# Kernel optimization log

Hardware: AMD Instinct MI355X
Metric: run time of the kernel (lower is better)

## Reference

```python
import jax, jax.numpy as jnp
import numpy as np

D = 64
H = 2          # n_heads
HD = D // H    # head_dim = 32
EPS = 1e-5


def _layer_norm(x, gamma, beta):
    mu = jnp.mean(x, axis=-1, keepdims=True)
    var = jnp.var(x, axis=-1, keepdims=True)
    return (x - mu) * jax.lax.rsqrt(var + EPS) * gamma + beta


def setup_inputs() -> dict:
    key = jax.random.key(0)
    ks = jax.random.split(key, 12)
    s = 0.05
    n_stocks, tau = 512, 512
    return {
        "x":     jax.random.normal(ks[0], (n_stocks, tau, D), dtype=jnp.float32),
        "Wqkv":  jax.random.normal(ks[1], (3 * D, D), dtype=jnp.float32) * s,
        "bqkv":  jax.random.normal(ks[2], (3 * D,), dtype=jnp.float32) * s,
        "Wo":    jax.random.normal(ks[3], (D, D), dtype=jnp.float32) * s,
        "bo":    jax.random.normal(ks[4], (D,), dtype=jnp.float32) * s,
        "g1":    jnp.ones((D,), dtype=jnp.float32),
        "beta1": jnp.zeros((D,), dtype=jnp.float32),
        "W1":    jax.random.normal(ks[5], (4 * D, D), dtype=jnp.float32) * s,
        "bf1":   jax.random.normal(ks[6], (4 * D,), dtype=jnp.float32) * s,
        "W2":    jax.random.normal(ks[7], (D, 4 * D), dtype=jnp.float32) * s,
        "bf2":   jax.random.normal(ks[8], (D,), dtype=jnp.float32) * s,
        "g2":    jnp.ones((D,), dtype=jnp.float32),
        "beta2": jnp.zeros((D,), dtype=jnp.float32),
    }


def reference(x, Wqkv, bqkv, Wo, bo, g1, beta1, W1, bf1, W2, bf2, g2, beta2):
    # x: (n_stocks, tau, D). The torch loop over tau == batched attention with
    # batch = tau, seq = n_stocks. Dropout is identity (eval mode).
    n_stocks, tau, d = x.shape
    Ht = jnp.transpose(x, (1, 0, 2))                    # (tau, S, D)

    qkv = Ht @ Wqkv.T + bqkv                            # (tau, S, 3D)
    q, k, v = jnp.split(qkv, 3, axis=-1)
    q = q.reshape(tau, n_stocks, H, HD)
    k = k.reshape(tau, n_stocks, H, HD)
    v = v.reshape(tau, n_stocks, H, HD)

    scores = jnp.einsum("bqhd,bkhd->bhqk", q, k) / jnp.sqrt(jnp.float32(HD))
    attn = jax.nn.softmax(scores, axis=-1)              # (tau, H, S, S)
    ctx = jnp.einsum("bhqk,bkhd->bqhd", attn, v).reshape(tau, n_stocks, D)
    attn_out = ctx @ Wo.T + bo                          # (tau, S, D)

    y = _layer_norm(attn_out + Ht, g1, beta1)           # residual + LN1
    ffn = jax.nn.relu(y @ W1.T + bf1) @ W2.T + bf2      # (tau, S, D)
    z = _layer_norm(ffn + y, g2, beta2)                 # residual + LN2

    return jnp.transpose(z, (1, 0, 2))                  # (n_stocks, tau, D)
```

## Files before the change

### kernel.cpp

```cpp
#include <hip/hip_runtime.h>
#include <hip/hip_bf16.h>
#include <cmath>

#define NS 512
#define NT 512
#define DIM 64
#define HD 32

typedef __attribute__((ext_vector_type(8))) short short8;
typedef __attribute__((ext_vector_type(16))) float f32x16;

union FragU { unsigned w[4]; short8 f; };

__device__ __forceinline__ float fexp2(float x) {
  float r; asm("v_exp_f32 %0, %1" : "=v"(r) : "v"(x)); return r;
}

__device__ __forceinline__ unsigned short bfbits(float x) {
  __hip_bfloat16 h = __float2bfloat16(x);
  return __builtin_bit_cast(unsigned short, h);
}
__device__ __forceinline__ unsigned pk2(float lo, float hi) {
  return (unsigned)bfbits(lo) | ((unsigned)bfbits(hi) << 16);
}
__device__ __forceinline__ float lo_f(unsigned w) { return __uint_as_float(w << 16); }
__device__ __forceinline__ float hi_f(unsigned w) { return __uint_as_float(w & 0xffff0000u); }
__device__ __forceinline__ short8 ldg8(const __hip_bfloat16* p) {
  return *reinterpret_cast<const short8*>(p);
}

__device__ __forceinline__ void pl32swap(unsigned& a, unsigned& b) {
  asm volatile("v_permlane32_swap_b32 %0, %1" : "+v"(a), "+v"(b));
}

__device__ __forceinline__ void repack(const float* p, short8& o1, short8& o2) {
  unsigned pk[8];
  #pragma unroll
  for (int j = 0; j < 8; ++j) pk[j] = pk2(p[2 * j], p[2 * j + 1]);
  pl32swap(pk[0], pk[2]);
  pl32swap(pk[1], pk[3]);
  pl32swap(pk[4], pk[6]);
  pl32swap(pk[5], pk[7]);
  FragU a1, a2;
  a1.w[0] = pk[0]; a1.w[1] = pk[1]; a1.w[2] = pk[2]; a1.w[3] = pk[3];
  a2.w[0] = pk[4]; a2.w[1] = pk[5]; a2.w[2] = pk[6]; a2.w[3] = pk[7];
  o1 = a1.f; o2 = a2.f;
}

__global__ void k_cvt(const float* __restrict__ Wqkv, const float* __restrict__ Wo,
                      const float* __restrict__ W1, const float* __restrict__ W2,
                      __hip_bfloat16* __restrict__ dst) {
  int i = blockIdx.x * 256 + threadIdx.x;
  float v;
  if (i < 12288) v = Wqkv[i];
  else if (i < 16384) v = Wo[i - 12288];
  else if (i < 32768) v = W1[i - 16384];
  else v = W2[i - 32768];
  dst[i] = __float2bfloat16(v);
}

__global__ __launch_bounds__(512, 4) void k_attn(
    const float* __restrict__ x, const __hip_bfloat16* __restrict__ Wb,
    const float* __restrict__ bqkv, __hip_bfloat16* __restrict__ ctx) {
  __shared__ char smem[65536];
  const int t = blockIdx.x, h = blockIdx.y;
  const int tid = threadIdx.x;
  const int l = tid & 63, wv = tid >> 6, hi = l >> 5, l31 = l & 31;

  short8 xf[2][4];
  #pragma unroll
  for (int rt = 0; rt < 2; ++rt) {
    int row = wv * 64 + rt * 32 + l31;
    const float* xr = x + ((size_t)row * NT + t) * DIM + hi * 8;
    #pragma unroll
    for (int st = 0; st < 4; ++st) {
      float4 f0 = *reinterpret_cast<const float4*>(xr + st * 16);
      float4 f1 = *reinterpret_cast<const float4*>(xr + st * 16 + 4);
      FragU fu;
      fu.w[0] = pk2(f0.x, f0.y); fu.w[1] = pk2(f0.z, f0.w);
      fu.w[2] = pk2(f1.x, f1.y); fu.w[3] = pk2(f1.z, f1.w);
      xf[rt][st] = fu.f;
    }
  }

  {
    short8 wkb[4];
    #pragma unroll
    for (int st = 0; st < 4; ++st)
      wkb[st] = ldg8(Wb + (size_t)(64 + h * 32 + l31) * 64 + st * 16 + hi * 8);
    #pragma unroll
    for (int rt = 0; rt < 2; ++rt) {
      f32x16 ka = {};
      #pragma unroll
      for (int st = 0; st < 4; ++st)
        ka = __builtin_amdgcn_mfma_f32_32x32x16_bf16(wkb[st], xf[rt][st], ka, 0, 0, 0);
      int stock = wv * 64 + rt * 32 + l31;
      char* kb = smem + stock * 64 + (hi << 3);
      #pragma unroll
      for (int rq = 0; rq < 4; ++rq) {
        uint2 d2 = make_uint2(pk2(ka[4 * rq + 0], ka[4 * rq + 1]),
                              pk2(ka[4 * rq + 2], ka[4 * rq + 3]));
        *reinterpret_cast<uint2*>(kb + ((rq ^ ((stock >> 1) & 3)) << 4)) = d2;
      }
    }
  }

  {
    short8 wvb[4];
    #pragma unroll
    for (int st = 0; st < 4; ++st)
      wvb[st] = ldg8(Wb + (size_t)(128 + h * 32 + l31) * 64 + st * 16 + hi * 8);
    #pragma unroll
    for (int rt = 0; rt < 2; ++rt) {
      f32x16 va = {};
      #pragma unroll
      for (int st = 0; st < 4; ++st)
        va = __builtin_amdgcn_mfma_f32_32x32x16_bf16(xf[rt][st], wvb[st], va, 0, 0, 0);
      #pragma unroll
      for (int g = 0; g < 4; ++g) {
        int kb = wv * 64 + rt * 32 + g * 8 + hi * 4;
        uint2 d2 = make_uint2(pk2(va[4 * g + 0], va[4 * g + 1]),
                              pk2(va[4 * g + 2], va[4 * g + 3]));
        *reinterpret_cast<uint2*>(
            smem + 32768 + l31 * 1024 + (((kb >> 3) ^ (l31 & 7)) << 4) + ((kb & 7) << 1)) = d2;
      }
    }
  }

  short8 qfrag[2][2];
  {
    short8 wqa[4];
    #pragma unroll
    for (int st = 0; st < 4; ++st)
      wqa[st] = ldg8(Wb + (size_t)(h * 32 + l31) * 64 + st * 16 + hi * 8);
    float bqv[16];
    #pragma unroll
    for (int r = 0; r < 16; ++r)
      bqv[r] = bqkv[h * 32 + (r & 3) + 8 * (r >> 2) + 4 * hi];
    #pragma unroll
    for (int rt = 0; rt < 2; ++rt) {
      f32x16 qa = {};
      #pragma unroll
      for (int st = 0; st < 4; ++st)
        qa = __builtin_amdgcn_mfma_f32_32x32x16_bf16(wqa[st], xf[rt][st], qa, 0, 0, 0);
      float p[16];
      #pragma unroll
      for (int r = 0; r < 16; ++r) p[r] = (qa[r] + bqv[r]) * 0.25503488921708395f;
      repack(p, qfrag[rt][0], qfrag[rt][1]);
    }
  }

  float bvv[16];
  #pragma unroll
  for (int r = 0; r < 16; ++r)
    bvv[r] = bqkv[128 + h * 32 + (r & 3) + 8 * (r >> 2) + 4 * hi];

  __syncthreads();

  f32x16 oacc[2], psum[2];
  #pragma unroll
  for (int i = 0; i < 16; ++i) {
    oacc[0][i] = 0.f; oacc[1][i] = 0.f;
    psum[0][i] = 0.f; psum[1][i] = 0.f;
  }

  #pragma clang loop unroll(disable)
  for (int kt = 0; kt < 16; ++kt) {
    short8 kfrag[2], vfrag[2];
    int row = kt * 32 + l31;
    #pragma unroll
    for (int dc = 0; dc < 2; ++dc)
      kfrag[dc] = *reinterpret_cast<const short8*>(
          smem + row * 64 + ((((dc << 1) | hi) ^ ((row >> 1) & 3)) << 4));
    #pragma unroll
    for (int c = 0; c < 2; ++c) {
      int ck = kt * 4 + (c << 1) + hi;
      vfrag[c] = *reinterpret_cast<const short8*>(
          smem + 32768 + l31 * 1024 + ((ck ^ (l31 & 7)) << 4));
    }
    #pragma unroll
    for (int sb = 0; sb < 2; ++sb) {
      f32x16 sC = {};
      sC = __builtin_amdgcn_mfma_f32_32x32x16_bf16(kfrag[0], qfrag[sb][0], sC, 0, 0, 0);
      sC = __builtin_amdgcn_mfma_f32_32x32x16_bf16(kfrag[1], qfrag[sb][1], sC, 0, 0, 0);
      float p[16];
      #pragma unroll
      for (int r = 0; r < 16; ++r) { p[r] = fexp2(sC[r]); psum[sb][r] += p[r]; }
      short8 a1, a2;
      repack(p, a1, a2);
      oacc[sb] = __builtin_amdgcn_mfma_f32_32x32x16_bf16(vfrag[0], a1, oacc[sb], 0, 0, 0);
      oacc[sb] = __builtin_amdgcn_mfma_f32_32x32x16_bf16(vfrag[1], a2, oacc[sb], 0, 0, 0);
    }
  }

  #pragma unroll
  for (int sb = 0; sb < 2; ++sb) {
    float s0 = ((psum[sb][0] + psum[sb][1]) + (psum[sb][2] + psum[sb][3]))
             + ((psum[sb][4] + psum[sb][5]) + (psum[sb][6] + psum[sb][7]));
    float s1 = ((psum[sb][8] + psum[sb][9]) + (psum[sb][10] + psum[sb][11]))
             + ((psum[sb][12] + psum[sb][13]) + (psum[sb][14] + psum[sb][15]));
    float ls = s0 + s1;
    float lt = ls + __shfl_xor(ls, 32, 64);
    float inv = 1.f / lt;
    int q = wv * 64 + sb * 32 + l31;
    __hip_bfloat16* cb = ctx + ((size_t)t * 512 + q) * 64 + h * 32;
    #pragma unroll
    for (int g = 0; g < 4; ++g) {
      uint2 d2 = make_uint2(
          pk2(fmaf(oacc[sb][4 * g + 0], inv, bvv[4 * g + 0]),
              fmaf(oacc[sb][4 * g + 1], inv, bvv[4 * g + 1])),
          pk2(fmaf(oacc[sb][4 * g + 2], inv, bvv[4 * g + 2]),
              fmaf(oacc[sb][4 * g + 3], inv, bvv[4 * g + 3])));
      *reinterpret_cast<uint2*>(cb + 8 * g + 4 * hi) = d2;
    }
  }
}

__global__ __launch_bounds__(512, 2) void k_tail(
    const __hip_bfloat16* __restrict__ ctx, const float* __restrict__ x,
    const __hip_bfloat16* __restrict__ Wob,
    const float* __restrict__ bo, const float* __restrict__ g1,
    const float* __restrict__ be1, const __hip_bfloat16* __restrict__ W1b,
    const float* __restrict__ bf1, const __hip_bfloat16* __restrict__ W2b,
    const float* __restrict__ bf2, const float* __restrict__ g2,
    const float* __restrict__ be2, float* __restrict__ out) {
  __shared__ char sm[133632];
  float* ps = reinterpret_cast<float*>(sm + 131072);
  const int t = blockIdx.x;
  const int tid = threadIdx.x;
  const int l = tid & 63, wv = tid >> 6, hi = l >> 5, l31 = l & 31;

  short8 wst[8];
  {
    const short8* w1p = reinterpret_cast<const short8*>(W1b);
    const short8* w2p = reinterpret_cast<const short8*>(W2b);
    #pragma unroll
    for (int j = 0; j < 4; ++j) wst[j] = w1p[tid + 512 * j];
    #pragma unroll
    for (int j = 0; j < 4; ++j) wst[4 + j] = w2p[tid + 512 * j];
  }

  {
    const short8* cp = reinterpret_cast<const short8*>(ctx + ((size_t)t * 512 + tid) * 64);
    #pragma unroll
    for (int c = 0; c < 8; ++c)
      *reinterpret_cast<short8*>(sm + tid * 128 + ((c ^ (tid & 7)) << 4)) = cp[c];
  }
  for (int i = tid; i < 640; i += 512) {
    float v;
    if (i < 64) v = g1[i];
    else if (i < 128) v = be1[i - 64];
    else if (i < 192) v = bo[i - 128];
    else if (i < 256) v = bf2[i - 192];
    else if (i < 320) v = g2[i - 256];
    else if (i < 384) v = be2[i - 320];
    else v = bf1[i - 384];
    ps[i] = v;
  }

  {
    short8 cb[2][4];
    #pragma unroll
    for (int stl = 0; stl < 2; ++stl) {
      int lr = wv * 64 + stl * 32 + l31;
      #pragma unroll
      for (int st = 0; st < 4; ++st)
        cb[stl][st] = *reinterpret_cast<const short8*>(
            sm + lr * 128 + ((((st << 1) | hi) ^ (lr & 7)) << 4));
    }
    #pragma unroll
    for (int dt = 0; dt < 2; ++dt) {
      short8 wa[4];
      #pragma unroll
      for (int st = 0; st < 4; ++st)
        wa[st] = ldg8(Wob + (size_t)(dt * 32 + l31) * 64 + st * 16 + hi * 8);
      #pragma unroll
      for (int stl = 0; stl < 2; ++stl) {
        f32x16 a = {};
        #pragma unroll
        for (int st = 0; st < 4; ++st)
          a = __builtin_amdgcn_mfma_f32_32x32x16_bf16(wa[st], cb[stl][st], a, 0, 0, 0);
        int lr = wv * 64 + stl * 32 + l31;
        #pragma unroll
        for (int q = 0; q < 4; ++q) {
          uint2 d2 = make_uint2(pk2(a[4 * q + 0], a[4 * q + 1]),
                                pk2(a[4 * q + 2], a[4 * q + 3]));
          *reinterpret_cast<uint2*>(
              sm + lr * 128 + (((dt * 4 + q) ^ (lr & 7)) << 4) + (hi << 3)) = d2;
        }
      }
    }
  }

  {
    #pragma unroll
    for (int j = 0; j < 4; ++j) {
      int g = tid + 512 * j;
      *reinterpret_cast<short8*>(
          sm + 65536 + (g >> 3) * 128 + (((g & 7) ^ ((g >> 3) & 7)) << 4)) = wst[j];
    }
    #pragma unroll
    for (int j = 0; j < 4; ++j) {
      int g = tid + 512 * j;
      *reinterpret_cast<short8*>(
          sm + 98304 + (g >> 5) * 512 + (((g & 31) ^ ((g >> 5) & 7)) << 4)) = wst[4 + j];
    }
  }
  __syncthreads();

  unsigned ypk[32];
  {
    float ao[64];
    #pragma unroll
    for (int c = 0; c < 8; ++c) {
      FragU fu;
      fu.f = *reinterpret_cast<const short8*>(sm + tid * 128 + ((c ^ (tid & 7)) << 4));
      #pragma unroll
      for (int u = 0; u < 4; ++u) {
        ao[c * 8 + 2 * u]     = lo_f(fu.w[u]);
        ao[c * 8 + 2 * u + 1] = hi_f(fu.w[u]);
      }
    }
    float y[64];
    const float4* xp = reinterpret_cast<const float4*>(x + ((size_t)tid * NT + t) * DIM);
    #pragma unroll
    for (int i = 0; i < 16; ++i) {
      float4 v = xp[i];
      y[4*i+0] = v.x + ao[4*i+0] + ps[128 + 4*i+0];
      y[4*i+1] = v.y + ao[4*i+1] + ps[128 + 4*i+1];
      y[4*i+2] = v.z + ao[4*i+2] + ps[128 + 4*i+2];
      y[4*i+3] = v.w + ao[4*i+3] + ps[128 + 4*i+3];
    }
    float m0 = 0.f, m1 = 0.f, m2 = 0.f, m3 = 0.f;
    #pragma unroll
    for (int j = 0; j < 16; ++j) {
      m0 += y[4*j+0]; m1 += y[4*j+1]; m2 += y[4*j+2]; m3 += y[4*j+3];
    }
    float mu = ((m0 + m1) + (m2 + m3)) * (1.f / 64.f);
    float v0 = 0.f, v1 = 0.f, v2 = 0.f, v3 = 0.f;
    #pragma unroll
    for (int j = 0; j < 16; ++j) {
      float t0 = y[4*j+0] - mu, t1 = y[4*j+1] - mu;
      float t2 = y[4*j+2] - mu, t3 = y[4*j+3] - mu;
      v0 = fmaf(t0, t0, v0); v1 = fmaf(t1, t1, v1);
      v2 = fmaf(t2, t2, v2); v3 = fmaf(t3, t3, v3);
    }
    float var = ((v0 + v1) + (v2 + v3)) * (1.f / 64.f);
    float rs = rsqrtf(var + 1e-5f);
    #pragma unroll
    for (int d = 0; d < 64; ++d) y[d] = (y[d] - mu) * rs * ps[d] + ps[64 + d];
    #pragma unroll
    for (int c = 0; c < 8; ++c) {
      FragU fu;
      #pragma unroll
      for (int u = 0; u < 4; ++u) {
        fu.w[u] = pk2(y[c*8 + 2*u], y[c*8 + 2*u + 1]);
        ypk[4 * c + u] = fu.w[u];
      }
      *reinterpret_cast<short8*>(sm + tid * 128 + ((c ^ (tid & 7)) << 4)) = fu.f;
    }
  }

  {
    short8 yb[2][4];
    #pragma unroll
    for (int stl = 0; stl < 2; ++stl) {
      int lr = wv * 64 + stl * 32 + l31;
      #pragma unroll
      for (int st = 0; st < 4; ++st)
        yb[stl][st] = *reinterpret_cast<const short8*>(
            sm + lr * 128 + ((((st << 1) | hi) ^ (lr & 7)) << 4));
    }
    f32x16 zacc[2][2];
    #pragma unroll
    for (int i = 0; i < 16; ++i) {
      zacc[0][0][i] = 0.f; zacc[0][1][i] = 0.f; zacc[1][0][i] = 0.f; zacc[1][1][i] = 0.f;
    }
    #pragma clang loop unroll_count(2)
    for (int jt = 0; jt < 8; ++jt) {
      short8 w1a[4];
      #pragma unroll
      for (int st = 0; st < 4; ++st) {
        int row = jt * 32 + l31, c1 = (st << 1) | hi;
        w1a[st] = *reinterpret_cast<const short8*>(
            sm + 65536 + row * 128 + ((c1 ^ (row & 7)) << 4));
      }
      short8 w2f[2][2];
      #pragma unroll
      for (int dt = 0; dt < 2; ++dt)
        #pragma unroll
        for (int ks = 0; ks < 2; ++ks) {
          int row = dt * 32 + l31, c2 = jt * 4 + ks * 2 + hi;
          w2f[dt][ks] = *reinterpret_cast<const short8*>(
              sm + 98304 + row * 512 + ((c2 ^ (row & 7)) << 4));
        }
      float b1v[16];
      #pragma unroll
      for (int r = 0; r < 16; ++r)
        b1v[r] = ps[384 + jt * 32 + (r & 3) + 8 * (r >> 2) + 4 * hi];
      #pragma unroll
      for (int stl = 0; stl < 2; ++stl) {
        f32x16 ha = {};
        #pragma unroll
        for (int st = 0; st < 4; ++st)
          ha = __builtin_amdgcn_mfma_f32_32x32x16_bf16(w1a[st], yb[stl][st], ha, 0, 0, 0);
        float p[16];
        #pragma unroll
        for (int r = 0; r < 16; ++r) p[r] = fmaxf(ha[r] + b1v[r], 0.f);
        short8 b1, b2;
        repack(p, b1, b2);
        zacc[0][stl] = __builtin_amdgcn_mfma_f32_32x32x16_bf16(w2f[0][0], b1, zacc[0][stl], 0, 0, 0);
        zacc[0][stl] = __builtin_amdgcn_mfma_f32_32x32x16_bf16(w2f[0][1], b2, zacc[0][stl], 0, 0, 0);
        zacc[1][stl] = __builtin_amdgcn_mfma_f32_32x32x16_bf16(w2f[1][0], b1, zacc[1][stl], 0, 0, 0);
        zacc[1][stl] = __builtin_amdgcn_mfma_f32_32x32x16_bf16(w2f[1][1], b2, zacc[1][stl], 0, 0, 0);
      }
    }
    #pragma unroll
    for (int dt = 0; dt < 2; ++dt)
      #pragma unroll
      for (int stl = 0; stl < 2; ++stl) {
        int lr = wv * 64 + stl * 32 + l31;
        #pragma unroll
        for (int q = 0; q < 4; ++q) {
          uint2 d2 = make_uint2(pk2(zacc[dt][stl][4 * q + 0], zacc[dt][stl][4 * q + 1]),
                                pk2(zacc[dt][stl][4 * q + 2], zacc[dt][stl][4 * q + 3]));
          *reinterpret_cast<uint2*>(
              sm + lr * 128 + (((dt * 4 + q) ^ (lr & 7)) << 4) + (hi << 3)) = d2;
        }
      }
  }

  {
    float z[64];
    #pragma unroll
    for (int c = 0; c < 8; ++c) {
      FragU zf;
      zf.f = *reinterpret_cast<const short8*>(sm + tid * 128 + ((c ^ (tid & 7)) << 4));
      #pragma unroll
      for (int u = 0; u < 4; ++u) {
        int d = c * 8 + 2 * u;
        z[d]     = lo_f(zf.w[u]) + ps[192 + d]     + lo_f(ypk[4 * c + u]);
        z[d + 1] = hi_f(zf.w[u]) + ps[192 + d + 1] + hi_f(ypk[4 * c + u]);
      }
    }
    float m0 = 0.f, m1 = 0.f, m2 = 0.f, m3 = 0.f;
    #pragma unroll
    for (int j = 0; j < 16; ++j) {
      m0 += z[4*j+0]; m1 += z[4*j+1]; m2 += z[4*j+2]; m3 += z[4*j+3];
    }
    float mu2 = ((m0 + m1) + (m2 + m3)) * (1.f / 64.f);
    float v0 = 0.f, v1 = 0.f, v2 = 0.f, v3 = 0.f;
    #pragma unroll
    for (int j = 0; j < 16; ++j) {
      float t0 = z[4*j+0] - mu2, t1 = z[4*j+1] - mu2;
      float t2 = z[4*j+2] - mu2, t3 = z[4*j+3] - mu2;
      v0 = fmaf(t0, t0, v0); v1 = fmaf(t1, t1, v1);
      v2 = fmaf(t2, t2, v2); v3 = fmaf(t3, t3, v3);
    }
    float var2 = ((v0 + v1) + (v2 + v3)) * (1.f / 64.f);
    float rs2 = rsqrtf(var2 + 1e-5f);
    float4* op = reinterpret_cast<float4*>(out + ((size_t)tid * NT + t) * DIM);
    #pragma unroll
    for (int i = 0; i < 16; ++i) {
      op[i] = make_float4(
          (z[4*i+0] - mu2) * rs2 * ps[256 + 4*i+0] + ps[320 + 4*i+0],
          (z[4*i+1] - mu2) * rs2 * ps[256 + 4*i+1] + ps[320 + 4*i+1],
          (z[4*i+2] - mu2) * rs2 * ps[256 + 4*i+2] + ps[320 + 4*i+2],
          (z[4*i+3] - mu2) * rs2 * ps[256 + 4*i+3] + ps[320 + 4*i+3]);
    }
  }
}

extern "C" void kernel_launch(void* const* d_in, const int* in_sizes, int n_in,
                              void* d_out, int out_size, void* d_ws, size_t ws_size,
                              hipStream_t stream) {
  const float* x    = (const float*)d_in[0];
  const float* Wqkv = (const float*)d_in[1];
  const float* bqkv = (const float*)d_in[2];
  const float* Wo   = (const float*)d_in[3];
  const float* bo   = (const float*)d_in[4];
  const float* g1   = (const float*)d_in[5];
  const float* be1  = (const float*)d_in[6];
  const float* W1   = (const float*)d_in[7];
  const float* bf1  = (const float*)d_in[8];
  const float* W2   = (const float*)d_in[9];
  const float* bf2  = (const float*)d_in[10];
  const float* g2   = (const float*)d_in[11];
  const float* be2  = (const float*)d_in[12];
  float* out = (float*)d_out;

  __hip_bfloat16* wb   = (__hip_bfloat16*)d_ws;
  __hip_bfloat16* ctxb = (__hip_bfloat16*)((char*)d_ws + 131072);

  hipLaunchKernelGGL(k_cvt, dim3(192), dim3(256), 0, stream, Wqkv, Wo, W1, W2, wb);
  hipLaunchKernelGGL(k_attn, dim3(NT, 2), dim3(512), 0, stream, x, wb, bqkv, ctxb);
  hipLaunchKernelGGL(k_tail, dim3(NT), dim3(512), 0, stream,
                     ctxb, x, wb + 12288, bo, g1, be1, wb + 16384, bf1,
                     wb + 32768, bf2, g2, be2, out);
}
```

Before: 152.6 us.

## Pre-convert x to bf16 fragment layout in separate kernel; scalar softmax sum

Adds a k_xpose kernel that converts x to bf16 once and stores it in MFMA fragment order. This lets both head blocks of k_attn load fragments with coalesced 16-byte reads instead of strided fp32 reads followed by per-head conversion. The per-element psum vector accumulators are replaced by a scalar running sum, which saves registers, and the inline-asm exp2 is swapped for the compiler builtin. In exchange there is an extra launch and an extra 32 MB bf16 write plus read through the workspace.

```diff
diff --git a/kernel.cpp b/kernel.cpp
--- a/kernel.cpp
+++ b/kernel.cpp
@@ -12,9 +12,11 @@
 
 union FragU { unsigned w[4]; short8 f; };
 
-__device__ __forceinline__ float fexp2(float x) {
-  float r; asm("v_exp_f32 %0, %1" : "=v"(r) : "v"(x)); return r;
-}
+#if __has_builtin(__builtin_amdgcn_exp2f)
+#define EXP2F __builtin_amdgcn_exp2f
+#else
+#define EXP2F exp2f
+#endif
 
 __device__ __forceinline__ unsigned short bfbits(float x) {
   __hip_bfloat16 h = __float2bfloat16(x);
@@ -59,8 +61,27 @@
   dst[i] = __float2bfloat16(v);
 }
 
+__global__ __launch_bounds__(512) void k_xpose(const float* __restrict__ x,
+                                               __hip_bfloat16* __restrict__ xb) {
+  const int t = blockIdx.x, s = threadIdx.x;
+  const int wv = s >> 6, rt = (s >> 5) & 1, l31 = s & 31;
+  const float* xr = x + ((size_t)s * NT + t) * DIM;
+  uint4* xo = reinterpret_cast<uint4*>(xb);
+  #pragma unroll
+  for (int st = 0; st < 4; ++st)
+    #pragma unroll
+    for (int hi = 0; hi < 2; ++hi) {
+      float4 a = *reinterpret_cast<const float4*>(xr + st * 16 + hi * 8);
+      float4 b = *reinterpret_cast<const float4*>(xr + st * 16 + hi * 8 + 4);
+      uint4 u = make_uint4(pk2(a.x, a.y), pk2(a.z, a.w),
+                           pk2(b.x, b.y), pk2(b.z, b.w));
+      size_t idx = ((((size_t)t * 2 + rt) * 4 + st) * 8 + wv) * 64 + hi * 32 + l31;
+      xo[idx] = u;
+    }
+}
+
 __global__ __launch_bounds__(512, 4) void k_attn(
-    const float* __restrict__ x, const __hip_bfloat16* __restrict__ Wb,
+    const __hip_bfloat16* __restrict__ xb, const __hip_bfloat16* __restrict__ Wb,
     const float* __restrict__ bqkv, __hip_bfloat16* __restrict__ ctx) {
   __shared__ char smem[65536];
   const int t = blockIdx.x, h = blockIdx.y;
@@ -68,19 +89,17 @@
   const int l = tid & 63, wv = tid >> 6, hi = l >> 5, l31 = l & 31;
 
   short8 xf[2][4];
-  #pragma unroll
-  for (int rt = 0; rt < 2; ++rt) {
-    int row = wv * 64 + rt * 32 + l31;
-    const float* xr = x + ((size_t)row * NT + t) * DIM + hi * 8;
-    #pragma unroll
-    for (int st = 0; st < 4; ++st) {
-      float4 f0 = *reinterpret_cast<const float4*>(xr + st * 16);
-      float4 f1 = *reinterpret_cast<const float4*>(xr + st * 16 + 4);
-      FragU fu;
-      fu.w[0] = pk2(f0.x, f0.y); fu.w[1] = pk2(f0.z, f0.w);
-      fu.w[2] = pk2(f1.x, f1.y); fu.w[3] = pk2(f1.z, f1.w);
-      xf[rt][st] = fu.f;
-    }
+  {
+    const uint4* xbp = reinterpret_cast<const uint4*>(xb);
+    #pragma unroll
+    for (int rt = 0; rt < 2; ++rt)
+      #pragma unroll
+      for (int st = 0; st < 4; ++st) {
+        uint4 u = xbp[((((size_t)t * 2 + rt) * 4 + st) * 8 + wv) * 64 + l];
+        FragU fu;
+        fu.w[0] = u.x; fu.w[1] = u.y; fu.w[2] = u.z; fu.w[3] = u.w;
+        xf[rt][st] = fu.f;
+      }
   }
 
   {
@@ -157,12 +176,10 @@
 
   __syncthreads();
 
-  f32x16 oacc[2], psum[2];
+  f32x16 oacc[2];
   #pragma unroll
-  for (int i = 0; i < 16; ++i) {
-    oacc[0][i] = 0.f; oacc[1][i] = 0.f;
-    psum[0][i] = 0.f; psum[1][i] = 0.f;
-  }
+  for (int i = 0; i < 16; ++i) { oacc[0][i] = 0.f; oacc[1][i] = 0.f; }
+  float lsum[2] = {0.f, 0.f};
 
   #pragma clang loop unroll(disable)
   for (int kt = 0; kt < 16; ++kt) {
@@ -185,7 +202,7 @@
       sC = __builtin_amdgcn_mfma_f32_32x32x16_bf16(kfrag[1], qfrag[sb][1], sC, 0, 0, 0);
       float p[16];
       #pragma unroll
-      for (int r = 0; r < 16; ++r) { p[r] = fexp2(sC[r]); psum[sb][r] += p[r]; }
+      for (int r = 0; r < 16; ++r) { p[r] = EXP2F(sC[r]); lsum[sb] += p[r]; }
       short8 a1, a2;
       repack(p, a1, a2);
       oacc[sb] = __builtin_amdgcn_mfma_f32_32x32x16_bf16(vfrag[0], a1, oacc[sb], 0, 0, 0);
@@ -195,12 +212,7 @@
 
   #pragma unroll
   for (int sb = 0; sb < 2; ++sb) {
-    float s0 = ((psum[sb][0] + psum[sb][1]) + (psum[sb][2] + psum[sb][3]))
-             + ((psum[sb][4] + psum[sb][5]) + (psum[sb][6] + psum[sb][7]));
-    float s1 = ((psum[sb][8] + psum[sb][9]) + (psum[sb][10] + psum[sb][11]))
-             + ((psum[sb][12] + psum[sb][13]) + (psum[sb][14] + psum[sb][15]));
-    float ls = s0 + s1;
-    float lt = ls + __shfl_xor(ls, 32, 64);
+    float lt = lsum[sb] + __shfl_xor(lsum[sb], 32, 64);
     float inv = 1.f / lt;
     int q = wv * 64 + sb * 32 + l31;
     __hip_bfloat16* cb = ctx + ((size_t)t * 512 + q) * 64 + h * 32;
@@ -490,10 +502,12 @@
   float* out = (float*)d_out;
 
   __hip_bfloat16* wb   = (__hip_bfloat16*)d_ws;
-  __hip_bfloat16* ctxb = (__hip_bfloat16*)((char*)d_ws + 131072);
+  __hip_bfloat16* xbb  = (__hip_bfloat16*)((char*)d_ws + 131072);
+  __hip_bfloat16* ctxb = (__hip_bfloat16*)((char*)d_ws + 131072 + 33554432);
 
   hipLaunchKernelGGL(k_cvt, dim3(192), dim3(256), 0, stream, Wqkv, Wo, W1, W2, wb);
-  hipLaunchKernelGGL(k_attn, dim3(NT, 2), dim3(512), 0, stream, x, wb, bqkv, ctxb);
+  hipLaunchKernelGGL(k_xpose, dim3(NT), dim3(512), 0, stream, x, xbb);
+  hipLaunchKernelGGL(k_attn, dim3(NT, 2), dim3(512), 0, stream, xbb, wb, bqkv, ctxb);
   hipLaunchKernelGGL(k_tail, dim3(NT), dim3(512), 0, stream,
                      ctxb, x, wb + 12288, bo, g1, be1, wb + 16384, bf1,
                      wb + 32768, bf2, g2, be2, out);
```

Result: no change. 151.6 us (-0.7%).
